# Optimization experiments

Measured on AMD Instinct MI355X. Metric: run time of the kernel, lower is better.

## Reference

```python
import jax, jax.numpy as jnp
import numpy as np

NEG_INF = -1e30  # stand-in for -inf pooling pad (matches torch max_pool2d implicit -inf pad)


def _max_pool(x, wh, ww, ph, pw):
    # x: (N, C, H, W); 'same'-style explicit padding as in torch max_pool2d
    return jax.lax.reduce_window(
        x, -jnp.inf, jax.lax.max,
        window_dimensions=(1, 1, wh, ww),
        window_strides=(1, 1, 1, 1),
        padding=((0, 0), (0, 0), (ph, ph), (pw, pw)))


def soft_erode(img):
    p1 = -_max_pool(-img, 3, 1, 1, 0)
    p2 = -_max_pool(-img, 1, 3, 0, 1)
    return jnp.minimum(p1, p2)


def soft_dilate(img):
    return _max_pool(img, 3, 3, 1, 1)


def soft_open(img):
    return soft_dilate(soft_erode(img))


def soft_skel(img, n_iter=50):
    skel = jax.nn.relu(img - soft_open(img))

    def body(carry, _):
        img, skel = carry
        img = soft_erode(img)
        delta = jax.nn.relu(img - soft_open(img))
        skel = skel + jax.nn.relu(delta - skel * delta)
        return (img, skel), None

    (_, skel), _ = jax.lax.scan(body, (img, skel), None, length=n_iter)
    return skel


def setup_inputs() -> dict:
    key = jax.random.key(0)
    k1, k2 = jax.random.split(key)
    N, C, H, W = 8, 1, 512, 512
    output = jax.random.normal(k1, (N, C, H, W), dtype=jnp.float32)
    target = jax.random.uniform(k2, (N, C, H, W), dtype=jnp.float32)
    return {"output": output, "target": target}


def reference(output, target):
    smooth = 1.0
    alpha = 0.7
    n_iter = 50
    axes = (1, 2, 3)  # per-sample reduction over C, H, W

    p = jax.nn.sigmoid(output)

    # soft clDice (vectorized over batch; original loops per sample with identical math)
    s_p = soft_skel(p, n_iter)
    s_l = soft_skel(target, n_iter)
    tprec = (jnp.sum(s_p * target, axes) + smooth) / (jnp.sum(s_p, axes) + smooth)
    tsens = (jnp.sum(s_l * p, axes) + smooth) / (jnp.sum(s_l, axes) + smooth)
    cl_dice = jnp.mean(1.0 - 2.0 * tprec * tsens / (tprec + tsens))

    # soft Dice
    inter = jnp.sum(p * target, axes)
    dice = jnp.mean(1.0 - 2.0 * (inter + smooth) /
                    (jnp.sum(p, axes) + jnp.sum(target, axes) + smooth))

    return alpha * dice + (1.0 - alpha) * cl_dice
```

## Files before the change

### kernel.cpp

```cpp
#include <hip/hip_runtime.h>
#include <math.h>

#define IMG   512
#define NSAMP 8
#define NIMG  16
#define PS    (IMG * IMG)

#define NBANDS 32
#define BH     (IMG / NBANDS)

__device__ __forceinline__ float sigm(float x) { return 1.0f / (1.0f + expf(-x)); }

__device__ __forceinline__ float dpp_a(float x) {
#if __has_builtin(__builtin_amdgcn_update_dpp)
    return __int_as_float(__builtin_amdgcn_update_dpp(0, __float_as_int(x),
                                                      0x130, 0xF, 0xF, true));
#else
    return __shfl_down(x, 1, 64);
#endif
}
__device__ __forceinline__ float dpp_b(float x) {
#if __has_builtin(__builtin_amdgcn_update_dpp)
    return __int_as_float(__builtin_amdgcn_update_dpp(0, __float_as_int(x),
                                                      0x138, 0xF, 0xF, true));
#else
    return __shfl_up(x, 1, 64);
#endif
}

__global__ __launch_bounds__(256) void prep_kernel(const float4* __restrict__ lg,
                                                   const float4* __restrict__ tg,
                                                   float4* __restrict__ X, int n4)
{
    int i = blockIdx.x * 256 + threadIdx.x;
    if (i < n4) {
        float4 L = lg[i];
        X[i]      = make_float4(sigm(L.x), sigm(L.y), sigm(L.z), sigm(L.w));
        X[i + n4] = tg[i];
    }
}

template<int C, bool ER, bool EC, bool INIT, bool LAST>
__device__ __forceinline__ void pipe_run(const float* __restrict__ xg,
                                         float* __restrict__ xo,
                                         float* __restrict__ Sg,
                                         int R0, int gcol, bool colOK, bool owned)
{
    const float INF = __builtin_inff();
    constexpr int RAW    = BH + 2 * C + 2;
    constexpr int INNER  = (C % 2 == 0) ? C : 2 * C;
    constexpr int NSTEPS = ((RAW + INNER - 1) / INNER) * INNER;
    constexpr int PAD    = NSTEPS - RAW;
    constexpr int T0PAR  = (C + 1 + PAD) & 1;
    constexpr int XS0    = 2 * C + 1 + PAD;
    constexpr int SS0    = 2 * C + 2 + PAD;
    const int t0 = R0 - C - 1 - PAD;

    float W[C][2], HM[C][2], SK[C], XQ[C], SQ[C];
    #pragma unroll
    for (int l = 0; l < C; ++l) {
        W[l][0] = INF;  W[l][1] = INF;
        HM[l][0] = -INF; HM[l][1] = -INF;
        SK[l] = 0.f;
    }

    const float* xp = xg + gcol;
    float* sp = Sg + gcol;
    float* op = xo + gcol;

    auto xld = [&](int r) -> float {
        if (ER || EC) {
            bool ok = (!ER || (unsigned)r < (unsigned)IMG) && (!EC || colOK);
            float v = INF;
            if (ok) v = xp[r * IMG];
            return v;
        }
        return xp[r * IMG];
    };
    auto sld = [&](int r) -> float {
        if (INIT) return 0.f;
        if (ER || EC) {
            bool ok = (!ER || (unsigned)r < (unsigned)IMG) && (!EC || colOK);
            float v = 0.f;
            if (ok) v = sp[r * IMG];
            return v;
        }
        return sp[r * IMG];
    };

    #pragma unroll
    for (int i = 0; i < C; ++i) XQ[i] = xld(t0 + i);
    #pragma unroll
    for (int i = 0; i < C; ++i) SQ[i] = INIT ? 0.f : sld(t0 - 1 + i);

    for (int kk = 0; kk < NSTEPS; kk += INNER) {
        #pragma unroll
        for (int j = 0; j < INNER; ++j) {
            const int k = kk + j;
            const int t = t0 + k;
            const int qi = j % C;
            float Cin = XQ[qi];
            XQ[qi] = xld(t + C);
            float snew = SQ[qi];
            if (!INIT) SQ[qi] = sld(t + C - 1);

            #pragma unroll
            for (int l = 0; l < C; ++l) {
                const int bp = (T0PAR + j + l + 1) & 1;
                float Acur = W[l][bp ^ 1];
                float Bcur = W[l][bp];
                float e = fminf(fminf(Acur, Cin), Bcur);
                e = fminf(e, dpp_a(Bcur));
                e = fminf(e, dpp_b(Bcur));
                if (ER) e = ((unsigned)(t - l - 1) < (unsigned)IMG) ? e : INF;
                float xd = e;
                if (EC) { xd = colOK ? e : -INF; e = colOK ? e : INF; }
                float hm = fmaxf(xd, fmaxf(dpp_a(xd), dpp_b(xd)));
                if (ER) hm = ((unsigned)(t - l - 1) < (unsigned)IMG) ? hm : -INF;
                float dil = fmaxf(fmaxf(HM[l][bp], HM[l][bp ^ 1]), hm);
                float d = fmaxf(Acur - dil, 0.f);
                const int si = (l + C - qi) % C;
                float skl = SK[si];
                SK[si] = (skl + d) - skl * d;
                W[l][bp ^ 1] = Cin;
                HM[l][bp] = hm;
                Cin = e;
            }

            if (!LAST) {
                if ((unsigned)(k - XS0) < BH) { if (owned) op[(t - C) * IMG] = Cin; }
            }
            if ((unsigned)(k - SS0) < BH) {
                const int so = (2 * C - 1 - qi) % C;
                if (owned) sp[(t - C - 1) * IMG] = SK[so];
            }
            SK[(C - ((j + 1) % C)) % C] = snew;
        }
    }
}

template<int C, bool INIT, bool LAST>
__global__ __launch_bounds__(256) void fused_pipe(const float* __restrict__ xin,
                                                  float* __restrict__ xout,
                                                  float* __restrict__ S)
{
    constexpr int OW = 64 - 2 * (C + 1);
    constexpr int NSTRIP = (IMG + OW - 1) / OW;
    const int lane = threadIdx.x & 63;
    const int task = blockIdx.x * 4 + (threadIdx.x >> 6);
    const int strip = task % NSTRIP;
    const int rem = task / NSTRIP;
    const int band = rem % NBANDS;
    const int img = rem / NBANDS;
    const int R0 = band * BH;
    const int gcol = strip * OW - (C + 1) + lane;
    const bool colOK = (unsigned)gcol < (unsigned)IMG;
    const bool owned = (lane >= C + 1) && (lane < C + 1 + OW) && colOK;
    const float* xg = xin + (size_t)img * PS;
    float* xo = xout + (size_t)img * PS;
    float* Sg = S + (size_t)img * PS;
    const bool erow = (band == 0) || (band == NBANDS - 1);
    const bool ecol = (strip == 0) || (strip * OW - (C + 1) + 63 >= IMG);

    if (erow) {
        if (ecol) pipe_run<C, true , true , INIT, LAST>(xg, xo, Sg, R0, gcol, colOK, owned);
        else      pipe_run<C, true , false, INIT, LAST>(xg, xo, Sg, R0, gcol, colOK, owned);
    } else {
        if (ecol) pipe_run<C, false, true , INIT, LAST>(xg, xo, Sg, R0, gcol, colOK, owned);
        else      pipe_run<C, false, false, INIT, LAST>(xg, xo, Sg, R0, gcol, colOK, owned);
    }
}

__global__ __launch_bounds__(256) void reduce_kernel(const float* __restrict__ logits,
                                                     const float* __restrict__ target,
                                                     const float* __restrict__ S,
                                                     float* __restrict__ partial)
{
    const int sample = blockIdx.y;
    const size_t base = (size_t)sample * PS;
    const float4* p4  = (const float4*)(logits + base);
    const float4* t4  = (const float4*)(target + base);
    const float4* sp4 = (const float4*)(S + base);
    const float4* sl4 = (const float4*)(S + (size_t)NSAMP * PS + base);
    float v[7] = {0.f, 0.f, 0.f, 0.f, 0.f, 0.f, 0.f};
    const int n4 = PS / 4;
    for (int i = blockIdx.x * 256 + threadIdx.x; i < n4; i += 32 * 256) {
        float4 L = p4[i], Tt = t4[i], SP = sp4[i], SL = sl4[i];
        float p;
        p = sigm(L.x); v[0] += SP.x * Tt.x; v[1] += SP.x; v[2] += SL.x * p; v[3] += SL.x; v[4] += p * Tt.x; v[5] += p; v[6] += Tt.x;
        p = sigm(L.y); v[0] += SP.y * Tt.y; v[1] += SP.y; v[2] += SL.y * p; v[3] += SL.y; v[4] += p * Tt.y; v[5] += p; v[6] += Tt.y;
        p = sigm(L.z); v[0] += SP.z * Tt.z; v[1] += SP.z; v[2] += SL.z * p; v[3] += SL.z; v[4] += p * Tt.z; v[5] += p; v[6] += Tt.z;
        p = sigm(L.w); v[0] += SP.w * Tt.w; v[1] += SP.w; v[2] += SL.w * p; v[3] += SL.w; v[4] += p * Tt.w; v[5] += p; v[6] += Tt.w;
    }
    #pragma unroll
    for (int off = 32; off > 0; off >>= 1)
        #pragma unroll
        for (int q = 0; q < 7; ++q) v[q] += __shfl_down(v[q], off);
    __shared__ float wred[4][7];
    int lane = threadIdx.x & 63, w = threadIdx.x >> 6;
    if (lane == 0)
        #pragma unroll
        for (int q = 0; q < 7; ++q) wred[w][q] = v[q];
    __syncthreads();
    if (threadIdx.x == 0) {
        #pragma unroll
        for (int q = 0; q < 7; ++q)
            partial[(sample * 32 + blockIdx.x) * 7 + q] =
                wred[0][q] + wred[1][q] + wred[2][q] + wred[3][q];
    }
}

__global__ __launch_bounds__(256) void final_kernel(const float* __restrict__ partial,
                                                    float* __restrict__ out)
{
    const int t = threadIdx.x;
    const int sample = t >> 5, part = t & 31;
    float v[7];
    #pragma unroll
    for (int q = 0; q < 7; ++q) v[q] = partial[(sample * 32 + part) * 7 + q];
    #pragma unroll
    for (int off = 16; off > 0; off >>= 1)
        #pragma unroll
        for (int q = 0; q < 7; ++q) v[q] += __shfl_down(v[q], off, 32);
    __shared__ float acc[NSAMP][7];
    if (part == 0)
        #pragma unroll
        for (int q = 0; q < 7; ++q) acc[sample][q] = v[q];
    __syncthreads();
    if (t == 0) {
        float cl = 0.f, dice = 0.f;
        for (int n = 0; n < NSAMP; n++) {
            float A = acc[n][0], Bv = acc[n][1], Cc = acc[n][2], D = acc[n][3];
            float E = acc[n][4], F = acc[n][5], G = acc[n][6];
            float tprec = (A + 1.0f) / (Bv + 1.0f);
            float tsens = (Cc + 1.0f) / (D + 1.0f);
            cl   += 1.0f - 2.0f * tprec * tsens / (tprec + tsens);
            dice += 1.0f - 2.0f * (E + 1.0f) / (F + G + 1.0f);
        }
        out[0] = 0.7f * (dice / NSAMP) + 0.3f * (cl / NSAMP);
    }
}

extern "C" void kernel_launch(void* const* d_in, const int* in_sizes, int n_in,
                              void* d_out, int out_size, void* d_ws, size_t ws_size,
                              hipStream_t stream)
{
    const float* logits = (const float*)d_in[0];
    const float* target = (const float*)d_in[1];
    float* out = (float*)d_out;

    const size_t NTOT = (size_t)NIMG * PS;
    float* Xa = (float*)d_ws;
    float* Xb = Xa + NTOT;
    float* S  = Xb + NTOT;
    float* partial = S + NTOT;

    const int n4 = (NSAMP * PS) / 4;
    prep_kernel<<<n4 / 256, 256, 0, stream>>>((const float4*)logits, (const float4*)target,
                                              (float4*)Xa, n4);

    const int B6 = 11 * NBANDS * NIMG / 4;
    const int B3 = 10 * NBANDS * NIMG / 4;
    fused_pipe<6, true , false><<<B6, 256, 0, stream>>>(Xa, Xb, S);
    fused_pipe<6, false, false><<<B6, 256, 0, stream>>>(Xb, Xa, S);
    fused_pipe<6, false, false><<<B6, 256, 0, stream>>>(Xa, Xb, S);
    fused_pipe<6, false, false><<<B6, 256, 0, stream>>>(Xb, Xa, S);
    fused_pipe<6, false, false><<<B6, 256, 0, stream>>>(Xa, Xb, S);
    fused_pipe<6, false, false><<<B6, 256, 0, stream>>>(Xb, Xa, S);
    fused_pipe<6, false, false><<<B6, 256, 0, stream>>>(Xa, Xb, S);
    fused_pipe<6, false, false><<<B6, 256, 0, stream>>>(Xb, Xa, S);
    fused_pipe<3, false, true ><<<B3, 256, 0, stream>>>(Xa, Xb, S);

    reduce_kernel<<<dim3(32, NSAMP), 256, 0, stream>>>(logits, target, S, partial);
    final_kernel<<<1, 256, 0, stream>>>(partial, out);
}
```

Before: 356.5 us.

## Process two columns per lane to shrink halo overhead in fused pipe

```diff
diff --git a/kernel.cpp b/kernel.cpp
--- a/kernel.cpp
+++ b/kernel.cpp
@@ -8,6 +8,9 @@
 
 #define NBANDS 32
 #define BH     (IMG / NBANDS)
+#define HALO   8
+#define OW     112
+#define NSTRIP 5
 
 __device__ __forceinline__ float sigm(float x) { return 1.0f / (1.0f + expf(-x)); }
 
@@ -44,7 +47,7 @@
 __device__ __forceinline__ void pipe_run(const float* __restrict__ xg,
                                          float* __restrict__ xo,
                                          float* __restrict__ Sg,
-                                         int R0, int gcol, bool colOK, bool owned)
+                                         int R0, int gc, bool colOK, bool owned)
 {
     const float INF = __builtin_inff();
     constexpr int RAW    = BH + 2 * C + 2;
@@ -56,42 +59,46 @@
     constexpr int SS0    = 2 * C + 2 + PAD;
     const int t0 = R0 - C - 1 - PAD;
 
-    float W[C][2], HM[C][2], SK[C], XQ[C], SQ[C];
+    float W0[C][2], W1[C][2], HM0[C][2], HM1[C][2];
+    float SK0[C], SK1[C], XQ0[C], XQ1[C], SQ0[C], SQ1[C];
     #pragma unroll
     for (int l = 0; l < C; ++l) {
-        W[l][0] = INF;  W[l][1] = INF;
-        HM[l][0] = -INF; HM[l][1] = -INF;
-        SK[l] = 0.f;
-    }
-
-    const float* xp = xg + gcol;
-    float* sp = Sg + gcol;
-    float* op = xo + gcol;
-
-    auto xld = [&](int r) -> float {
+        W0[l][0] = INF;  W0[l][1] = INF;  W1[l][0] = INF;  W1[l][1] = INF;
+        HM0[l][0] = -INF; HM0[l][1] = -INF; HM1[l][0] = -INF; HM1[l][1] = -INF;
+        SK0[l] = 0.f; SK1[l] = 0.f;
+    }
+
+    const float* xp = xg + gc;
+    float* sp = Sg + gc;
+    float* op = xo + gc;
+
+    auto xld = [&](int r) -> float2 {
         if (ER || EC) {
             bool ok = (!ER || (unsigned)r < (unsigned)IMG) && (!EC || colOK);
-            float v = INF;
-            if (ok) v = xp[r * IMG];
+            float2 v = make_float2(INF, INF);
+            if (ok) v = *(const float2*)(xp + r * IMG);
             return v;
         }
-        return xp[r * IMG];
+        return *(const float2*)(xp + r * IMG);
     };
-    auto sld = [&](int r) -> float {
-        if (INIT) return 0.f;
+    auto sld = [&](int r) -> float2 {
+        if (INIT) return make_float2(0.f, 0.f);
         if (ER || EC) {
             bool ok = (!ER || (unsigned)r < (unsigned)IMG) && (!EC || colOK);
-            float v = 0.f;
-            if (ok) v = sp[r * IMG];
+            float2 v = make_float2(0.f, 0.f);
+            if (ok) v = *(const float2*)(sp + r * IMG);
             return v;
         }
-        return sp[r * IMG];
+        return *(const float2*)(sp + r * IMG);
     };
 
     #pragma unroll
-    for (int i = 0; i < C; ++i) XQ[i] = xld(t0 + i);
-    #pragma unroll
-    for (int i = 0; i < C; ++i) SQ[i] = INIT ? 0.f : sld(t0 - 1 + i);
+    for (int i = 0; i < C; ++i) { float2 v = xld(t0 + i); XQ0[i] = v.x; XQ1[i] = v.y; }
+    #pragma unroll
+    for (int i = 0; i < C; ++i) {
+        float2 v = INIT ? make_float2(0.f, 0.f) : sld(t0 - 1 + i);
+        SQ0[i] = v.x; SQ1[i] = v.y;
+    }
 
     for (int kk = 0; kk < NSTEPS; kk += INNER) {
         #pragma unroll
@@ -99,42 +106,58 @@
             const int k = kk + j;
             const int t = t0 + k;
             const int qi = j % C;
-            float Cin = XQ[qi];
-            XQ[qi] = xld(t + C);
-            float snew = SQ[qi];
-            if (!INIT) SQ[qi] = sld(t + C - 1);
+            float Cin0 = XQ0[qi], Cin1 = XQ1[qi];
+            { float2 nv = xld(t + C); XQ0[qi] = nv.x; XQ1[qi] = nv.y; }
+            float sn0 = SQ0[qi], sn1 = SQ1[qi];
+            if (!INIT) { float2 sv = sld(t + C - 1); SQ0[qi] = sv.x; SQ1[qi] = sv.y; }
 
             #pragma unroll
             for (int l = 0; l < C; ++l) {
                 const int bp = (T0PAR + j + l + 1) & 1;
-                float Acur = W[l][bp ^ 1];
-                float Bcur = W[l][bp];
-                float e = fminf(fminf(Acur, Cin), Bcur);
-                e = fminf(e, dpp_a(Bcur));
-                e = fminf(e, dpp_b(Bcur));
-                if (ER) e = ((unsigned)(t - l - 1) < (unsigned)IMG) ? e : INF;
-                float xd = e;
-                if (EC) { xd = colOK ? e : -INF; e = colOK ? e : INF; }
-                float hm = fmaxf(xd, fmaxf(dpp_a(xd), dpp_b(xd)));
-                if (ER) hm = ((unsigned)(t - l - 1) < (unsigned)IMG) ? hm : -INF;
-                float dil = fmaxf(fmaxf(HM[l][bp], HM[l][bp ^ 1]), hm);
-                float d = fmaxf(Acur - dil, 0.f);
+                float A0 = W0[l][bp ^ 1], B0 = W0[l][bp];
+                float A1 = W1[l][bp ^ 1], B1 = W1[l][bp];
+                float e0 = fminf(fminf(A0, Cin0), B0);
+                float e1 = fminf(fminf(A1, Cin1), B1);
+                e0 = fminf(e0, fminf(dpp_b(B1), B1));
+                e1 = fminf(e1, fminf(B0, dpp_a(B0)));
+                if (ER) {
+                    bool rok = (unsigned)(t - l - 1) < (unsigned)IMG;
+                    e0 = rok ? e0 : INF;  e1 = rok ? e1 : INF;
+                }
+                float xd0 = e0, xd1 = e1;
+                if (EC) {
+                    xd0 = colOK ? e0 : -INF;  e0 = colOK ? e0 : INF;
+                    xd1 = colOK ? e1 : -INF;  e1 = colOK ? e1 : INF;
+                }
+                float hm0 = fmaxf(fmaxf(dpp_b(xd1), xd0), xd1);
+                float hm1 = fmaxf(fmaxf(xd0, xd1), dpp_a(xd0));
+                if (ER) {
+                    bool rok = (unsigned)(t - l - 1) < (unsigned)IMG;
+                    hm0 = rok ? hm0 : -INF;  hm1 = rok ? hm1 : -INF;
+                }
+                float dil0 = fmaxf(fmaxf(HM0[l][bp], HM0[l][bp ^ 1]), hm0);
+                float dil1 = fmaxf(fmaxf(HM1[l][bp], HM1[l][bp ^ 1]), hm1);
+                float d0 = fmaxf(A0 - dil0, 0.f);
+                float d1 = fmaxf(A1 - dil1, 0.f);
                 const int si = (l + C - qi) % C;
-                float skl = SK[si];
-                SK[si] = (skl + d) - skl * d;
-                W[l][bp ^ 1] = Cin;
-                HM[l][bp] = hm;
-                Cin = e;
+                float s0 = SK0[si]; SK0[si] = (s0 + d0) - s0 * d0;
+                float s1 = SK1[si]; SK1[si] = (s1 + d1) - s1 * d1;
+                W0[l][bp ^ 1] = Cin0;  W1[l][bp ^ 1] = Cin1;
+                HM0[l][bp] = hm0;      HM1[l][bp] = hm1;
+                Cin0 = e0;  Cin1 = e1;
             }
 
             if (!LAST) {
-                if ((unsigned)(k - XS0) < BH) { if (owned) op[(t - C) * IMG] = Cin; }
+                if ((unsigned)(k - XS0) < BH) {
+                    if (owned) *(float2*)(op + (t - C) * IMG) = make_float2(Cin0, Cin1);
+                }
             }
             if ((unsigned)(k - SS0) < BH) {
                 const int so = (2 * C - 1 - qi) % C;
-                if (owned) sp[(t - C - 1) * IMG] = SK[so];
+                if (owned) *(float2*)(sp + (t - C - 1) * IMG) = make_float2(SK0[so], SK1[so]);
             }
-            SK[(C - ((j + 1) % C)) % C] = snew;
+            const int ins = (C - ((j + 1) % C)) % C;
+            SK0[ins] = sn0;  SK1[ins] = sn1;
         }
     }
 }
@@ -144,8 +167,6 @@
                                                   float* __restrict__ xout,
                                                   float* __restrict__ S)
 {
-    constexpr int OW = 64 - 2 * (C + 1);
-    constexpr int NSTRIP = (IMG + OW - 1) / OW;
     const int lane = threadIdx.x & 63;
     const int task = blockIdx.x * 4 + (threadIdx.x >> 6);
     const int strip = task % NSTRIP;
@@ -153,21 +174,21 @@
     const int band = rem % NBANDS;
     const int img = rem / NBANDS;
     const int R0 = band * BH;
-    const int gcol = strip * OW - (C + 1) + lane;
-    const bool colOK = (unsigned)gcol < (unsigned)IMG;
-    const bool owned = (lane >= C + 1) && (lane < C + 1 + OW) && colOK;
+    const int gc = strip * OW - HALO + 2 * lane;
+    const bool colOK = (unsigned)gc < (unsigned)IMG;
+    const bool owned = (lane >= HALO / 2) && (lane < 64 - HALO / 2) && colOK;
     const float* xg = xin + (size_t)img * PS;
     float* xo = xout + (size_t)img * PS;
     float* Sg = S + (size_t)img * PS;
     const bool erow = (band == 0) || (band == NBANDS - 1);
-    const bool ecol = (strip == 0) || (strip * OW - (C + 1) + 63 >= IMG);
+    const bool ecol = (strip == 0) || (strip * OW - HALO + 127 >= IMG);
 
     if (erow) {
-        if (ecol) pipe_run<C, true , true , INIT, LAST>(xg, xo, Sg, R0, gcol, colOK, owned);
-        else      pipe_run<C, true , false, INIT, LAST>(xg, xo, Sg, R0, gcol, colOK, owned);
+        if (ecol) pipe_run<C, true , true , INIT, LAST>(xg, xo, Sg, R0, gc, colOK, owned);
+        else      pipe_run<C, true , false, INIT, LAST>(xg, xo, Sg, R0, gc, colOK, owned);
     } else {
-        if (ecol) pipe_run<C, false, true , INIT, LAST>(xg, xo, Sg, R0, gcol, colOK, owned);
-        else      pipe_run<C, false, false, INIT, LAST>(xg, xo, Sg, R0, gcol, colOK, owned);
+        if (ecol) pipe_run<C, false, true , INIT, LAST>(xg, xo, Sg, R0, gc, colOK, owned);
+        else      pipe_run<C, false, false, INIT, LAST>(xg, xo, Sg, R0, gc, colOK, owned);
     }
 }
 
@@ -259,17 +280,16 @@
     prep_kernel<<<n4 / 256, 256, 0, stream>>>((const float4*)logits, (const float4*)target,
                                               (float4*)Xa, n4);
 
-    const int B6 = 11 * NBANDS * NIMG / 4;
-    const int B3 = 10 * NBANDS * NIMG / 4;
-    fused_pipe<6, true , false><<<B6, 256, 0, stream>>>(Xa, Xb, S);
-    fused_pipe<6, false, false><<<B6, 256, 0, stream>>>(Xb, Xa, S);
-    fused_pipe<6, false, false><<<B6, 256, 0, stream>>>(Xa, Xb, S);
-    fused_pipe<6, false, false><<<B6, 256, 0, stream>>>(Xb, Xa, S);
-    fused_pipe<6, false, false><<<B6, 256, 0, stream>>>(Xa, Xb, S);
-    fused_pipe<6, false, false><<<B6, 256, 0, stream>>>(Xb, Xa, S);
-    fused_pipe<6, false, false><<<B6, 256, 0, stream>>>(Xa, Xb, S);
-    fused_pipe<6, false, false><<<B6, 256, 0, stream>>>(Xb, Xa, S);
-    fused_pipe<3, false, true ><<<B3, 256, 0, stream>>>(Xa, Xb, S);
+    const int B = NSTRIP * NBANDS * NIMG / 4;
+    fused_pipe<6, true , false><<<B, 256, 0, stream>>>(Xa, Xb, S);
+    fused_pipe<6, false, false><<<B, 256, 0, stream>>>(Xb, Xa, S);
+    fused_pipe<6, false, false><<<B, 256, 0, stream>>>(Xa, Xb, S);
+    fused_pipe<6, false, false><<<B, 256, 0, stream>>>(Xb, Xa, S);
+    fused_pipe<6, false, false><<<B, 256, 0, stream>>>(Xa, Xb, S);
+    fused_pipe<6, false, false><<<B, 256, 0, stream>>>(Xb, Xa, S);
+    fused_pipe<6, false, false><<<B, 256, 0, stream>>>(Xa, Xb, S);
+    fused_pipe<6, false, false><<<B, 256, 0, stream>>>(Xb, Xa, S);
+    fused_pipe<3, false, true ><<<B, 256, 0, stream>>>(Xa, Xb, S);
 
     reduce_kernel<<<dim3(32, NSAMP), 256, 0, stream>>>(logits, target, S, partial);
     final_kernel<<<1, 256, 0, stream>>>(partial, out);
```

New measurement: 477.1 us. 33.8% more time.
